# Kernel optimization log

Hardware: AMD Instinct MI355X
Metric: run time of the kernel (lower is better)

The kernel has to match this reference:

```python
import jax, jax.numpy as jnp
import numpy as np

EPS = 1e-8  # torch F.cosine_similarity norm clamp
TEMPERATURE = 0.05


def setup_inputs() -> dict:
    key = jax.random.key(0)
    k1, k2 = jax.random.split(key)
    N, D = 8192, 768
    query_embeddings = jax.random.normal(k1, (N, D), dtype=jnp.float32)
    content_embeddings = jax.random.normal(k2, (N, D), dtype=jnp.float32)
    return {"query_embeddings": query_embeddings, "content_embeddings": content_embeddings}


def reference(query_embeddings, content_embeddings):
    # cosine_similarity(q[:,None], c[None,:], dim=2) == normalize(q) @ normalize(c).T
    qn = query_embeddings / jnp.maximum(
        jnp.linalg.norm(query_embeddings, axis=-1, keepdims=True), EPS)
    cn = content_embeddings / jnp.maximum(
        jnp.linalg.norm(content_embeddings, axis=-1, keepdims=True), EPS)
    sim = jnp.einsum('nd,md->nm', qn, cn) / TEMPERATURE  # [N, N]
    # cross-entropy with targets = arange(N): positive is the diagonal
    logz = jax.nn.logsumexp(sim, axis=-1)                # [N]
    loss = jnp.mean(logz - jnp.diagonal(sim))
    return loss
```

## Files before the change

### kernel.cpp

```cpp
#include <hip/hip_runtime.h>
#include <hip/hip_bf16.h>


#define NROWS 8192
#define DDIM  768
#define BM 128
#define BN 128
#define BK 64
#define NT (NROWS / BN)
#define TILES_K (DDIM / BK)

constexpr float INV_TEMP = 20.0f;
constexpr float NORM_EPS = 1e-8f;

using bf16 = __hip_bfloat16;
typedef __attribute__((ext_vector_type(4))) float  f32x4;
typedef __attribute__((ext_vector_type(8))) short  bf16x8;

__global__ void normalize_kernel(const float* __restrict__ q,
                                 const float* __restrict__ c,
                                 bf16* __restrict__ qn, bf16* __restrict__ cn,
                                 float* __restrict__ invq, float* __restrict__ invc) {
    int row = blockIdx.x;
    const float* src;
    bf16* dst;
    float* invp;
    if (row < NROWS) {
        src = q + (size_t)row * DDIM; dst = qn + (size_t)row * DDIM; invp = invq + row;
    } else {
        int r = row - NROWS;
        src = c + (size_t)r * DDIM; dst = cn + (size_t)r * DDIM; invp = invc + r;
    }
    int t = threadIdx.x;
    float v0 = src[t], v1 = src[t + 256], v2 = src[t + 512];
    float ss = v0 * v0 + v1 * v1 + v2 * v2;
    #pragma unroll
    for (int m = 32; m; m >>= 1) ss += __shfl_xor(ss, m);
    __shared__ float wsum[4];
    if ((t & 63) == 0) wsum[t >> 6] = ss;
    __syncthreads();
    float tot = wsum[0] + wsum[1] + wsum[2] + wsum[3];
    float inv = 1.0f / fmaxf(sqrtf(tot), NORM_EPS);
    if (t == 0) *invp = inv;
    dst[t]       = __float2bfloat16(v0 * inv);
    dst[t + 256] = __float2bfloat16(v1 * inv);
    dst[t + 512] = __float2bfloat16(v2 * inv);
}

__global__ void diag_kernel(const float* __restrict__ q, const float* __restrict__ c,
                            const float* __restrict__ invq, const float* __restrict__ invc,
                            float* __restrict__ diag) {
    int wid = threadIdx.x >> 6, lane = threadIdx.x & 63;
    int row = blockIdx.x * 4 + wid;
    const float* qr = q + (size_t)row * DDIM;
    const float* cr = c + (size_t)row * DDIM;
    float dot = 0.f;
    #pragma unroll
    for (int j = 0; j < DDIM / 64; ++j) dot += qr[lane + j * 64] * cr[lane + j * 64];
    #pragma unroll
    for (int m = 32; m; m >>= 1) dot += __shfl_xor(dot, m);
    if (lane == 0) diag[row] = dot * invq[row] * invc[row] * INV_TEMP;
}

__device__ __forceinline__ void async_copy16(bf16* lds_dst, const bf16* g_src) {
    __builtin_amdgcn_global_load_lds(
        (const __attribute__((address_space(1))) void*)g_src,
        (__attribute__((address_space(3))) void*)lds_dst,
        16, 0, 0);
}

__global__ void simgemm_kernel(const bf16* __restrict__ A, const bf16* __restrict__ B,
                               float* __restrict__ partial) {
    __shared__ bf16 Alds[BM][BK];
    __shared__ bf16 Blds[BN][BK];
    __shared__ float red[BM][2];

    int bid = blockIdx.x;
    int tm = bid / NT, tn = bid % NT;
    int rowBase = tm * BM, colBase = tn * BN;
    int tid = threadIdx.x;
    int wid = tid >> 6, lane = tid & 63;
    int wr = wid >> 1, wc = wid & 1;

    f32x4 acc[4][4] = {};

    const int srow = wid * 32 + (lane >> 3);
    const int scol = (lane & 7) * 8;
    const bf16* ag = A + (size_t)(rowBase + srow) * DDIM + scol;
    const bf16* bg = B + (size_t)(colBase + srow) * DDIM + scol;
    bf16* alb = &Alds[wid * 32][0];
    bf16* blb = &Blds[wid * 32][0];

    for (int kt = 0; kt < TILES_K; ++kt) {
        int k0 = kt * BK;
        #pragma unroll
        for (int j = 0; j < 4; ++j) {
            async_copy16(alb + j * 8 * BK, ag + (size_t)j * 8 * DDIM + k0);
            async_copy16(blb + j * 8 * BK, bg + (size_t)j * 8 * DDIM + k0);
        }
        __syncthreads();

        #pragma unroll
        for (int kk = 0; kk < BK; kk += 32) {
            const int kele = kk + (lane >> 4) * 8;
            const int arow = wr * 64 + (lane & 15);
            const int brow = wc * 64 + (lane & 15);
            bf16x8 afrag[4], bfrag[4];
            #pragma unroll
            for (int m = 0; m < 4; ++m)
                afrag[m] = *(const bf16x8*)&Alds[arow + m * 16][kele];
            #pragma unroll
            for (int n = 0; n < 4; ++n)
                bfrag[n] = *(const bf16x8*)&Blds[brow + n * 16][kele];
            #pragma unroll
            for (int m = 0; m < 4; ++m)
                #pragma unroll
                for (int n = 0; n < 4; ++n)
                    acc[m][n] = __builtin_amdgcn_mfma_f32_16x16x32_bf16(
                        afrag[m], bfrag[n], acc[m][n], 0, 0, 0);
        }
        __syncthreads();
    }

    #pragma unroll
    for (int m = 0; m < 4; ++m) {
        float rs[4];
        #pragma unroll
        for (int r = 0; r < 4; ++r) {
            float s = 0.f;
            #pragma unroll
            for (int n = 0; n < 4; ++n)
                s += __expf(fmaf(INV_TEMP, acc[m][n][r], -INV_TEMP));
            s += __shfl_xor(s, 1);
            s += __shfl_xor(s, 2);
            s += __shfl_xor(s, 4);
            s += __shfl_xor(s, 8);
            rs[r] = s;
        }
        if ((lane & 15) == 0) {
            int rgrp = lane >> 4;
            #pragma unroll
            for (int r = 0; r < 4; ++r)
                red[wr * 64 + m * 16 + rgrp * 4 + r][wc] = rs[r];
        }
    }
    __syncthreads();
    if (tid < BM) {
        float s = red[tid][0] + red[tid][1];
        partial[(size_t)(rowBase + tid) * NT + tn] = s;
    }
}

__global__ void finalize_kernel(const float* __restrict__ partial,
                                const float* __restrict__ diag,
                                float* __restrict__ out) {
    int row = blockIdx.x * 256 + threadIdx.x;
    const float4* p = (const float4*)(partial + (size_t)row * NT);
    float z = 0.f;
    #pragma unroll
    for (int i = 0; i < NT / 4; ++i) {
        float4 v = p[i];
        z += v.x + v.y + v.z + v.w;
    }
    float term = INV_TEMP + logf(z) - diag[row];
    #pragma unroll
    for (int m = 32; m; m >>= 1) term += __shfl_xor(term, m);
    __shared__ float wsum[4];
    if ((threadIdx.x & 63) == 0) wsum[threadIdx.x >> 6] = term;
    __syncthreads();
    if (threadIdx.x == 0) {
        float s = wsum[0] + wsum[1] + wsum[2] + wsum[3];
        atomicAdd(out, s * (1.0f / NROWS));
    }
}

extern "C" void kernel_launch(void* const* d_in, const int* in_sizes, int n_in,
                              void* d_out, int out_size, void* d_ws, size_t ws_size,
                              hipStream_t stream) {
    const float* q = (const float*)d_in[0];
    const float* c = (const float*)d_in[1];
    float* out = (float*)d_out;

    char* ws = (char*)d_ws;
    bf16* qn = (bf16*)ws;
    bf16* cn = (bf16*)(ws + (size_t)NROWS * DDIM * 2);
    float* invq = (float*)(ws + (size_t)NROWS * DDIM * 4);
    float* invc = invq + NROWS;
    float* diag = invc + NROWS;
    float* partial = diag + NROWS;

    hipMemsetAsync(d_out, 0, sizeof(float), stream);

    normalize_kernel<<<2 * NROWS, 256, 0, stream>>>(q, c, qn, cn, invq, invc);
    diag_kernel<<<NROWS / 4, 256, 0, stream>>>(q, c, invq, invc, diag);
    simgemm_kernel<<<(NROWS / BM) * (NROWS / BN), 256, 0, stream>>>(qn, cn, partial);
    finalize_kernel<<<NROWS / 256, 256, 0, stream>>>(partial, diag, out);
}
```

Baseline: 224.3 us.

## Rewrite GEMM as double-buffered 256x256 pipelined kernel and fuse norm/diag

The similarity GEMM moves to 256x256 tiles with 512 threads and a double-buffered LDS pipeline. It uses swizzled layouts to avoid bank conflicts, interleaves async global-to-LDS copies with MFMA quarters, and adds explicit waitcnt, barrier and priority control. The normalize and diagonal kernels are fused into one vectorized pass that reads q and c once. The aim is to raise MFMA utilization and cut launch and memory traffic, at the cost of 128KB of LDS per block, which may exceed the per-CU budget at two blocks per CU, plus fragile hand scheduling.

```diff
diff --git a/kernel.cpp b/kernel.cpp
--- a/kernel.cpp
+++ b/kernel.cpp
@@ -4,11 +4,12 @@
 
 #define NROWS 8192
 #define DDIM  768
-#define BM 128
-#define BN 128
+#define ROWB  1536
+#define FROWB 3072
 #define BK 64
-#define NT (NROWS / BN)
-#define TILES_K (DDIM / BK)
+#define NKT  (DDIM / BK)
+#define NIT  (NKT / 2)
+#define GRID_T (NROWS / 256)
 
 constexpr float INV_TEMP = 20.0f;
 constexpr float NORM_EPS = 1e-8f;
@@ -17,114 +18,162 @@
 typedef __attribute__((ext_vector_type(4))) float  f32x4;
 typedef __attribute__((ext_vector_type(8))) short  bf16x8;
 
-__global__ void normalize_kernel(const float* __restrict__ q,
-                                 const float* __restrict__ c,
+__global__ void norm_diag_kernel(const float* __restrict__ q, const float* __restrict__ c,
                                  bf16* __restrict__ qn, bf16* __restrict__ cn,
-                                 float* __restrict__ invq, float* __restrict__ invc) {
-    int row = blockIdx.x;
-    const float* src;
-    bf16* dst;
-    float* invp;
-    if (row < NROWS) {
-        src = q + (size_t)row * DDIM; dst = qn + (size_t)row * DDIM; invp = invq + row;
-    } else {
-        int r = row - NROWS;
-        src = c + (size_t)r * DDIM; dst = cn + (size_t)r * DDIM; invp = invc + r;
-    }
-    int t = threadIdx.x;
-    float v0 = src[t], v1 = src[t + 256], v2 = src[t + 512];
-    float ss = v0 * v0 + v1 * v1 + v2 * v2;
-    #pragma unroll
-    for (int m = 32; m; m >>= 1) ss += __shfl_xor(ss, m);
-    __shared__ float wsum[4];
-    if ((t & 63) == 0) wsum[t >> 6] = ss;
-    __syncthreads();
-    float tot = wsum[0] + wsum[1] + wsum[2] + wsum[3];
-    float inv = 1.0f / fmaxf(sqrtf(tot), NORM_EPS);
-    if (t == 0) *invp = inv;
-    dst[t]       = __float2bfloat16(v0 * inv);
-    dst[t + 256] = __float2bfloat16(v1 * inv);
-    dst[t + 512] = __float2bfloat16(v2 * inv);
-}
-
-__global__ void diag_kernel(const float* __restrict__ q, const float* __restrict__ c,
-                            const float* __restrict__ invq, const float* __restrict__ invc,
-                            float* __restrict__ diag) {
-    int wid = threadIdx.x >> 6, lane = threadIdx.x & 63;
-    int row = blockIdx.x * 4 + wid;
-    const float* qr = q + (size_t)row * DDIM;
-    const float* cr = c + (size_t)row * DDIM;
-    float dot = 0.f;
-    #pragma unroll
-    for (int j = 0; j < DDIM / 64; ++j) dot += qr[lane + j * 64] * cr[lane + j * 64];
-    #pragma unroll
-    for (int m = 32; m; m >>= 1) dot += __shfl_xor(dot, m);
-    if (lane == 0) diag[row] = dot * invq[row] * invc[row] * INV_TEMP;
-}
-
-__device__ __forceinline__ void async_copy16(bf16* lds_dst, const bf16* g_src) {
+                                 float* __restrict__ diag) {
+    int row = blockIdx.x, t = threadIdx.x;
+    const float4* qv = (const float4*)(q + (size_t)row * DDIM);
+    const float4* cv = (const float4*)(c + (size_t)row * DDIM);
+    float4 a = qv[t], b = cv[t];
+    float ssq = a.x * a.x + a.y * a.y + a.z * a.z + a.w * a.w;
+    float ssc = b.x * b.x + b.y * b.y + b.z * b.z + b.w * b.w;
+    float dot = a.x * b.x + a.y * b.y + a.z * b.z + a.w * b.w;
+    #pragma unroll
+    for (int m = 32; m; m >>= 1) {
+        ssq += __shfl_xor(ssq, m);
+        ssc += __shfl_xor(ssc, m);
+        dot += __shfl_xor(dot, m);
+    }
+    __shared__ float w3[3][4];
+    if ((t & 63) == 0) { w3[t >> 6][0] = ssq; w3[t >> 6][1] = ssc; w3[t >> 6][2] = dot; }
+    __syncthreads();
+    float SSQ = w3[0][0] + w3[1][0] + w3[2][0];
+    float SSC = w3[0][1] + w3[1][1] + w3[2][1];
+    float DOT = w3[0][2] + w3[1][2] + w3[2][2];
+    float invq = 1.0f / fmaxf(sqrtf(SSQ), NORM_EPS);
+    float invc = 1.0f / fmaxf(sqrtf(SSC), NORM_EPS);
+    if (t == 0) diag[row] = DOT * invq * invc * INV_TEMP;
+    union { ushort4 u; bf16 h[4]; } oq, oc;
+    oq.h[0] = __float2bfloat16(a.x * invq); oq.h[1] = __float2bfloat16(a.y * invq);
+    oq.h[2] = __float2bfloat16(a.z * invq); oq.h[3] = __float2bfloat16(a.w * invq);
+    oc.h[0] = __float2bfloat16(b.x * invc); oc.h[1] = __float2bfloat16(b.y * invc);
+    oc.h[2] = __float2bfloat16(b.z * invc); oc.h[3] = __float2bfloat16(b.w * invc);
+    ((ushort4*)(qn + (size_t)row * DDIM))[t] = oq.u;
+    ((ushort4*)(cn + (size_t)row * DDIM))[t] = oc.u;
+}
+
+__device__ __forceinline__ void async16(void* l, const void* g) {
     __builtin_amdgcn_global_load_lds(
-        (const __attribute__((address_space(1))) void*)g_src,
-        (__attribute__((address_space(3))) void*)lds_dst,
-        16, 0, 0);
-}
-
+        (const __attribute__((address_space(1))) void*)g,
+        (__attribute__((address_space(3))) void*)l, 16, 0, 0);
+}
+
+#define BARRIER __builtin_amdgcn_s_barrier()
+#define SCHED0  __builtin_amdgcn_sched_barrier(0)
+#define PRIO1   __builtin_amdgcn_s_setprio(1)
+#define PRIO0   __builtin_amdgcn_s_setprio(0)
+#define LGKM0   do { asm volatile("s_waitcnt lgkmcnt(0)" ::: "memory"); SCHED0; } while (0)
+#define VMCNT(n) do { asm volatile("s_waitcnt vmcnt(" #n ")" ::: "memory"); SCHED0; } while (0)
+
+#define STAGE_A(P, H, KT) do {                                              \
+    const char* _g = aG + (size_t)(H) * 128 * ROWB + (size_t)(KT) * 128;    \
+    char* _l = lds + (P) * 65536 + (H) * 16384 + dstW;                      \
+    async16(_l, _g);                                                        \
+    async16(_l + 8192, _g + 64 * ROWB);                                     \
+} while (0)
+#define STAGE_B(P, H, KT) do {                                              \
+    const char* _g = bG + (size_t)(H) * 128 * ROWB + (size_t)(KT) * 128;    \
+    char* _l = lds + 32768 + (P) * 65536 + (H) * 16384 + dstW;              \
+    async16(_l, _g);                                                        \
+    async16(_l + 8192, _g + 64 * ROWB);                                     \
+} while (0)
+
+#define READ_A(P, MH) do {                                                  \
+    const char* _ab = lds + (P) * 65536 + aBaseT + (MH) * 64 * 128;         \
+    _Pragma("unroll") for (int mi = 0; mi < 4; ++mi) {                      \
+        a[mi][0] = *(const bf16x8*)(_ab + mi * 2048 + xk0);                 \
+        a[mi][1] = *(const bf16x8*)(_ab + mi * 2048 + xk1);                 \
+    }                                                                       \
+} while (0)
+#define READ_B(P, NH) do {                                                  \
+    const char* _bb = lds + 32768 + (P) * 65536 + bBaseT + (NH) * 32 * 128; \
+    _Pragma("unroll") for (int ni = 0; ni < 2; ++ni) {                      \
+        bfr[NH][ni][0] = *(const bf16x8*)(_bb + ni * 2048 + xk0);           \
+        bfr[NH][ni][1] = *(const bf16x8*)(_bb + ni * 2048 + xk1);           \
+    }                                                                       \
+} while (0)
+
+#define MFMA_Q(MH, NH)                                                      \
+    _Pragma("unroll") for (int mi = 0; mi < 4; ++mi)                        \
+    _Pragma("unroll") for (int ni = 0; ni < 2; ++ni) {                      \
+        acc[(MH)*4+mi][(NH)*2+ni] = __builtin_amdgcn_mfma_f32_16x16x32_bf16(\
+            a[mi][0], bfr[NH][ni][0], acc[(MH)*4+mi][(NH)*2+ni], 0, 0, 0);  \
+        acc[(MH)*4+mi][(NH)*2+ni] = __builtin_amdgcn_mfma_f32_16x16x32_bf16(\
+            a[mi][1], bfr[NH][ni][1], acc[(MH)*4+mi][(NH)*2+ni], 0, 0, 0);  \
+    }
+
+__launch_bounds__(512, 2)
 __global__ void simgemm_kernel(const bf16* __restrict__ A, const bf16* __restrict__ B,
                                float* __restrict__ partial) {
-    __shared__ bf16 Alds[BM][BK];
-    __shared__ bf16 Blds[BN][BK];
-    __shared__ float red[BM][2];
-
-    int bid = blockIdx.x;
-    int tm = bid / NT, tn = bid % NT;
-    int rowBase = tm * BM, colBase = tn * BN;
-    int tid = threadIdx.x;
-    int wid = tid >> 6, lane = tid & 63;
-    int wr = wid >> 1, wc = wid & 1;
-
-    f32x4 acc[4][4] = {};
-
-    const int srow = wid * 32 + (lane >> 3);
-    const int scol = (lane & 7) * 8;
-    const bf16* ag = A + (size_t)(rowBase + srow) * DDIM + scol;
-    const bf16* bg = B + (size_t)(colBase + srow) * DDIM + scol;
-    bf16* alb = &Alds[wid * 32][0];
-    bf16* blb = &Blds[wid * 32][0];
-
-    for (int kt = 0; kt < TILES_K; ++kt) {
-        int k0 = kt * BK;
-        #pragma unroll
-        for (int j = 0; j < 4; ++j) {
-            async_copy16(alb + j * 8 * BK, ag + (size_t)j * 8 * DDIM + k0);
-            async_copy16(blb + j * 8 * BK, bg + (size_t)j * 8 * DDIM + k0);
-        }
-        __syncthreads();
-
-        #pragma unroll
-        for (int kk = 0; kk < BK; kk += 32) {
-            const int kele = kk + (lane >> 4) * 8;
-            const int arow = wr * 64 + (lane & 15);
-            const int brow = wc * 64 + (lane & 15);
-            bf16x8 afrag[4], bfrag[4];
-            #pragma unroll
-            for (int m = 0; m < 4; ++m)
-                afrag[m] = *(const bf16x8*)&Alds[arow + m * 16][kele];
-            #pragma unroll
-            for (int n = 0; n < 4; ++n)
-                bfrag[n] = *(const bf16x8*)&Blds[brow + n * 16][kele];
-            #pragma unroll
-            for (int m = 0; m < 4; ++m)
-                #pragma unroll
-                for (int n = 0; n < 4; ++n)
-                    acc[m][n] = __builtin_amdgcn_mfma_f32_16x16x32_bf16(
-                        afrag[m], bfrag[n], acc[m][n], 0, 0, 0);
-        }
-        __syncthreads();
-    }
-
-    #pragma unroll
-    for (int m = 0; m < 4; ++m) {
-        float rs[4];
+    __shared__ __attribute__((aligned(16))) char smem[131072];
+    char* lds = smem;
+
+    const int bid = blockIdx.x;
+    const int tm = bid >> 5, tn = bid & 31;
+    const int rowBase = tm * 256, colBase = tn * 256;
+    const int tid = threadIdx.x;
+    const int wid = tid >> 6, lane = tid & 63;
+    const int wr = wid >> 2, wc = wid & 3;
+
+    const int sr  = tid >> 3;
+    const int scb = ((tid & 7) * 16) ^ ((sr & 7) << 4);
+    const char* aG = (const char*)A + (size_t)(rowBase + sr) * ROWB + scb;
+    const char* bG = (const char*)B + (size_t)(colBase + sr) * ROWB + scb;
+    const int dstW = wid * 1024;
+
+    const int aBaseT = wr * 16384 + (lane & 15) * 128;
+    const int bBaseT = (wc >> 1) * 16384 + ((wc & 1) * 64 + (lane & 15)) * 128;
+    const int klane  = (lane >> 4) * 16;
+    const int swz    = (lane & 7) << 4;
+    const int xk0    = klane ^ swz;
+    const int xk1    = (64 + klane) ^ swz;
+
+    f32x4  acc[8][4] = {};
+    bf16x8 a[4][2];
+    bf16x8 bfr[2][2][2];
+
+    STAGE_A(0, 0, 0); STAGE_A(0, 1, 0);
+    STAGE_B(0, 0, 0); STAGE_B(0, 1, 0);
+    STAGE_A(1, 0, 1); STAGE_A(1, 1, 1);
+    VMCNT(4);
+    BARRIER; SCHED0;
+
+    for (int i = 0; i < NIT; ++i) {
+        const int t1 = 2 * i + 1;
+        const int t2 = 2 * i + 2, t3 = 2 * i + 3;
+        const bool more = (i + 1 < NIT);
+        READ_A(0, 0); READ_B(0, 0);
+        STAGE_B(1, 0, t1);
+        BARRIER; LGKM0; PRIO1; MFMA_Q(0, 0); PRIO0; BARRIER; SCHED0;
+        READ_B(0, 1);
+        STAGE_B(1, 1, t1);
+        BARRIER; LGKM0; PRIO1; MFMA_Q(0, 1); PRIO0; BARRIER; SCHED0;
+        READ_A(0, 1);
+        if (more) STAGE_A(0, 0, t2);
+        BARRIER; LGKM0; PRIO1; MFMA_Q(1, 0); PRIO0; BARRIER; SCHED0;
+        if (more) STAGE_A(0, 1, t2);
+        BARRIER; LGKM0; PRIO1; MFMA_Q(1, 1); PRIO0;
+        if (more) { VMCNT(4); } else { VMCNT(0); }
+        BARRIER; SCHED0;
+        READ_A(1, 0); READ_B(1, 0);
+        if (more) STAGE_B(0, 0, t2);
+        BARRIER; LGKM0; PRIO1; MFMA_Q(0, 0); PRIO0; BARRIER; SCHED0;
+        READ_B(1, 1);
+        if (more) STAGE_B(0, 1, t2);
+        BARRIER; LGKM0; PRIO1; MFMA_Q(0, 1); PRIO0; BARRIER; SCHED0;
+        READ_A(1, 1);
+        if (more) STAGE_A(1, 0, t3);
+        BARRIER; LGKM0; PRIO1; MFMA_Q(1, 0); PRIO0; BARRIER; SCHED0;
+        if (more) STAGE_A(1, 1, t3);
+        BARRIER; LGKM0; PRIO1; MFMA_Q(1, 1); PRIO0;
+        if (more) { VMCNT(4); }
+        BARRIER; SCHED0;
+    }
+
+    __syncthreads();
+    float* red = (float*)smem;
+    #pragma unroll
+    for (int m = 0; m < 8; ++m) {
         #pragma unroll
         for (int r = 0; r < 4; ++r) {
             float s = 0.f;
@@ -135,30 +184,24 @@
             s += __shfl_xor(s, 2);
             s += __shfl_xor(s, 4);
             s += __shfl_xor(s, 8);
-            rs[r] = s;
+            if ((lane & 15) == 0)
+                red[(wr * 128 + m * 16 + (lane >> 4) * 4 + r) * 4 + wc] = s;
         }
-        if ((lane & 15) == 0) {
-            int rgrp = lane >> 4;
-            #pragma unroll
-            for (int r = 0; r < 4; ++r)
-                red[wr * 64 + m * 16 + rgrp * 4 + r][wc] = rs[r];
-        }
-    }
-    __syncthreads();
-    if (tid < BM) {
-        float s = red[tid][0] + red[tid][1];
-        partial[(size_t)(rowBase + tid) * NT + tn] = s;
-    }
+    }
+    __syncthreads();
+    if (tid < 256)
+        partial[(size_t)(rowBase + tid) * GRID_T + tn] =
+            red[tid * 4 + 0] + red[tid * 4 + 1] + red[tid * 4 + 2] + red[tid * 4 + 3];
 }
 
 __global__ void finalize_kernel(const float* __restrict__ partial,
                                 const float* __restrict__ diag,
                                 float* __restrict__ out) {
     int row = blockIdx.x * 256 + threadIdx.x;
-    const float4* p = (const float4*)(partial + (size_t)row * NT);
+    const float4* p = (const float4*)(partial + (size_t)row * GRID_T);
     float z = 0.f;
     #pragma unroll
-    for (int i = 0; i < NT / 4; ++i) {
+    for (int i = 0; i < GRID_T / 4; ++i) {
         float4 v = p[i];
         z += v.x + v.y + v.z + v.w;
     }
@@ -184,15 +227,12 @@
     char* ws = (char*)d_ws;
     bf16* qn = (bf16*)ws;
     bf16* cn = (bf16*)(ws + (size_t)NROWS * DDIM * 2);
-    float* invq = (float*)(ws + (size_t)NROWS * DDIM * 4);
-    float* invc = invq + NROWS;
-    float* diag = invc + NROWS;
+    float* diag = (float*)(ws + (size_t)NROWS * DDIM * 4);
     float* partial = diag + NROWS;
 
     hipMemsetAsync(d_out, 0, sizeof(float), stream);
 
-    normalize_kernel<<<2 * NROWS, 256, 0, stream>>>(q, c, qn, cn, invq, invc);
-    diag_kernel<<<NROWS / 4, 256, 0, stream>>>(q, c, invq, invc, diag);
-    simgemm_kernel<<<(NROWS / BM) * (NROWS / BN), 256, 0, stream>>>(qn, cn, partial);
+    norm_diag_kernel<<<NROWS, 192, 0, stream>>>(q, c, qn, cn, diag);
+    simgemm_kernel<<<GRID_T * GRID_T, 512, 0, stream>>>(qn, cn, partial);
     finalize_kernel<<<NROWS / 256, 256, 0, stream>>>(partial, diag, out);
 }
```

After: 193.3 us. 13.8% less time.
